# Performance work log

Measured on AMD Instinct MI355X. Metric: run time of the kernel, lower is better.

Reference implementation:

```python
import jax, jax.numpy as jnp
import numpy as np

B, S, D_IN, D_OUT = 8, 2048, 4096, 4096
RANK, N_ADAPTERS = 16, 8


def setup_inputs() -> dict:
    key = jax.random.key(0)
    k = jax.random.split(key, 6)
    x = jax.random.normal(k[0], (B, S, D_IN), dtype=jnp.float32)
    W = jax.random.normal(k[1], (D_OUT, D_IN), dtype=jnp.float32) * 0.02
    bias = jax.random.normal(k[2], (D_OUT,), dtype=jnp.float32) * 0.02
    lora_a = jax.random.normal(k[3], (N_ADAPTERS, RANK, D_IN), dtype=jnp.float32) * 0.02
    lora_b = jax.random.normal(k[4], (N_ADAPTERS, D_OUT, RANK), dtype=jnp.float32) * 0.02
    adapter_indices = jax.random.randint(k[5], (B,), 0, N_ADAPTERS, dtype=jnp.int64)
    return {"x": x, "W": W, "bias": bias, "lora_a": lora_a,
            "lora_b": lora_b, "adapter_indices": adapter_indices}


def reference(x, W, bias, lora_a, lora_b, adapter_indices):
    # Base linear: y = x @ W.T + bias
    base = jnp.einsum('bsi,oi->bso', x, W) + bias
    # Per-batch-element adapter gather (adapter index is shared across the seq dim)
    a = lora_a[adapter_indices]            # [B, r, D_in]
    b = lora_b[adapter_indices]            # [B, D_out, r]
    inter = jnp.einsum('bsi,bri->bsr', x, a)      # x_group @ a_i.T
    lora_out = jnp.einsum('bsr,bor->bso', inter, b)  # intermediate @ b_i.T
    return base + lora_out
```

## Files before the change

### kernel.cpp

```cpp
#include <hip/hip_runtime.h>


#define DIN     4096
#define DOUT    4096
#define RANK    16
#define M_DIM   16384
#define K_DIM   DIN
#define N_DIM   DOUT
#define BK      64
#define NT      (K_DIM / BK)
#define LDS_BYTES 131072

typedef __attribute__((ext_vector_type(8))) short  short8;
typedef __attribute__((ext_vector_type(4))) float  floatx4;
typedef __attribute__((ext_vector_type(4))) unsigned int uintx4;

__device__ __forceinline__ unsigned short f2bf(float f) {
  union { float f; unsigned int u; } v; v.f = f;
  return (unsigned short)((v.u + 0x7FFFu + ((v.u >> 16) & 1u)) >> 16);
}
__device__ __forceinline__ unsigned int pk2(float a, float b) {
  return (unsigned int)f2bf(a) | ((unsigned int)f2bf(b) << 16);
}

__device__ __forceinline__ int load_adapter(const int* __restrict__ p, int b) {
  bool i64 = (p[1] == 0) & (p[3] == 0) & (p[5] == 0) & (p[7] == 0);
  return i64 ? p[2 * b] : p[b];
}

__device__ __forceinline__ void async16(const unsigned short* g, void* s) {
  __builtin_amdgcn_global_load_lds(
      (const __attribute__((address_space(1))) void*)g,
      (__attribute__((address_space(3))) void*)s, 16, 0, 0);
}

__global__ __launch_bounds__(256) void conv_stream(const float* __restrict__ w,
                                                   unsigned short* __restrict__ wbf) {
  size_t base = ((size_t)blockIdx.x * 256 + threadIdx.x) * 8;
  const floatx4* src = (const floatx4*)(w + base);
  floatx4 f0 = __builtin_nontemporal_load(src);
  floatx4 f1 = __builtin_nontemporal_load(src + 1);
  uintx4 p;
  p.x = pk2(f0.x, f0.y); p.y = pk2(f0.z, f0.w);
  p.z = pk2(f1.x, f1.y); p.w = pk2(f1.z, f1.w);
  *(uintx4*)(wbf + base) = p;
}

__global__ __launch_bounds__(256) void inter16(
    const unsigned short* __restrict__ xbf,
    const float* __restrict__ lora_a,
    const int* __restrict__ adapters,
    float* __restrict__ inter) {
  __shared__ floatx4 red[4][64];
  const int tid = threadIdx.x, wave = tid >> 6, lane = tid & 63;
  const int fr = lane & 15, fq = lane >> 4;
  const int row0 = blockIdx.x * 16;
  const int adapter = load_adapter(adapters, row0 >> 11);
  const unsigned short* xp = xbf + (size_t)(row0 + fr) * DIN;
  const float* ap = lora_a + ((size_t)adapter * RANK + fr) * DIN;
  floatx4 acc = {};
  const int kbeg = blockIdx.y * 2048 + wave * 512;
#pragma unroll 2
  for (int k0 = kbeg; k0 < kbeg + 512; k0 += 32) {
    const int k = k0 + fq * 8;
    short8 xf = *(const short8*)(xp + k);
    floatx4 b0 = *(const floatx4*)(ap + k);
    floatx4 b1 = *(const floatx4*)(ap + k + 4);
    uintx4 bpk;
    bpk.x = pk2(b0.x, b0.y); bpk.y = pk2(b0.z, b0.w);
    bpk.z = pk2(b1.x, b1.y); bpk.w = pk2(b1.z, b1.w);
    acc = __builtin_amdgcn_mfma_f32_16x16x32_bf16(xf, *(short8*)&bpk, acc, 0, 0, 0);
  }
  red[wave][lane] = acc;
  __syncthreads();
  if (wave == 0) {
    floatx4 s = red[0][lane] + red[1][lane] + red[2][lane] + red[3][lane];
#pragma unroll
    for (int j = 0; j < 4; ++j)
      atomicAdd(&inter[(size_t)(row0 + fq * 4 + j) * RANK + fr], s[j]);
  }
}

#define PHASE_END() do {                                    \
    __builtin_amdgcn_sched_barrier(0);                      \
    __builtin_amdgcn_s_barrier();                           \
    __builtin_amdgcn_sched_barrier(0); } while (0)

__global__ __launch_bounds__(512, 2) void gemm256(
    const unsigned short* __restrict__ A,
    const unsigned short* __restrict__ Bw,
    const float* __restrict__ bias,
    const float* __restrict__ inter,
    const float* __restrict__ lora_b,
    const int* __restrict__ adapters,
    float* __restrict__ out) {
  extern __shared__ char lds[];
  const int tid  = threadIdx.x;
  const int lane = tid & 63, wave = tid >> 6;
  const int wm = wave >> 2, wn = wave & 3;

  const int wg   = ((int)blockIdx.x & 7) * 128 + ((int)blockIdx.x >> 3);
  const int row0 = (wg >> 4) * 256;
  const int col0 = (wg & 15) * 256;

  const int sg = (lane & 7) ^ (lane >> 3);
  const int sr = wave * 16 + (lane >> 3);
  const unsigned short* pA0 = A  + (size_t)(row0 + sr) * K_DIM + sg * 8;
  const unsigned short* pB0 = Bw + (size_t)(col0 + sr) * K_DIM + sg * 8;
  char* const dA0 = lds + wave * 2048;

#define STG_A(h, kt, buf) do {                                            \
    const unsigned short* _p = pA0 + (size_t)(h) * 128 * K_DIM + (kt) * BK; \
    char* _d = dA0 + (buf) * 65536 + (h) * 16384;                         \
    async16(_p, _d);                                                      \
    async16(_p + (size_t)8 * K_DIM, _d + 1024); } while (0)
#define STG_B(h, kt, buf) do {                                            \
    const unsigned short* _p = pB0 + (size_t)(h) * 128 * K_DIM + (kt) * BK; \
    char* _d = dA0 + 32768 + (buf) * 65536 + (h) * 16384;                 \
    async16(_p, _d);                                                      \
    async16(_p + (size_t)8 * K_DIM, _d + 1024); } while (0)

  const int fr = lane & 15, fq = lane >> 4;
  const int swz = (fr & 7) << 4;
  const int kb0 = (fq * 16) ^ swz;
  const int kb1 = (64 + fq * 16) ^ swz;
  const int ar = wm * 64 + fr;
  const int br = wn * 32 + fr;

  floatx4 acc[8][4] = {};
  short8 a[4][2], bl[2][2], bh[2][2];

  STG_A(0, 0, 0); STG_B(0, 0, 0); STG_B(1, 0, 0); STG_A(1, 0, 0);
  STG_A(0, 1, 1); STG_B(0, 1, 1); STG_B(1, 1, 1);
  asm volatile("s_waitcnt vmcnt(6)" ::: "memory");
  __builtin_amdgcn_sched_barrier(0);
  __builtin_amdgcn_s_barrier();
  __builtin_amdgcn_sched_barrier(0);

  for (int t = 0; t < NT; ++t) {
    const int buf = t & 1, nbuf = buf ^ 1;
    const char* ab = lds + buf * 65536;
    const char* bb = ab + 32768;
#pragma unroll
    for (int mt = 0; mt < 4; ++mt) {
      a[mt][0] = *(const short8*)(ab + (ar + mt * 16) * 128 + kb0);
      a[mt][1] = *(const short8*)(ab + (ar + mt * 16) * 128 + kb1);
    }
#pragma unroll
    for (int nt = 0; nt < 2; ++nt) {
      bl[nt][0] = *(const short8*)(bb + (br + nt * 16) * 128 + kb0);
      bl[nt][1] = *(const short8*)(bb + (br + nt * 16) * 128 + kb1);
    }
    if (t + 1 < NT) STG_A(1, t + 1, nbuf);
    __builtin_amdgcn_s_setprio(1);
#pragma unroll
    for (int mt = 0; mt < 4; ++mt)
#pragma unroll
      for (int nt = 0; nt < 2; ++nt) {
        acc[mt][nt] = __builtin_amdgcn_mfma_f32_16x16x32_bf16(a[mt][0], bl[nt][0], acc[mt][nt], 0, 0, 0);
        acc[mt][nt] = __builtin_amdgcn_mfma_f32_16x16x32_bf16(a[mt][1], bl[nt][1], acc[mt][nt], 0, 0, 0);
      }
    __builtin_amdgcn_s_setprio(0);
    PHASE_END();
#pragma unroll
    for (int nt = 0; nt < 2; ++nt) {
      bh[nt][0] = *(const short8*)(bb + (128 + br + nt * 16) * 128 + kb0);
      bh[nt][1] = *(const short8*)(bb + (128 + br + nt * 16) * 128 + kb1);
    }
    if (t + 2 < NT) STG_A(0, t + 2, buf);
    __builtin_amdgcn_s_setprio(1);
#pragma unroll
    for (int mt = 0; mt < 4; ++mt)
#pragma unroll
      for (int nt = 0; nt < 2; ++nt) {
        acc[mt][2 + nt] = __builtin_amdgcn_mfma_f32_16x16x32_bf16(a[mt][0], bh[nt][0], acc[mt][2 + nt], 0, 0, 0);
        acc[mt][2 + nt] = __builtin_amdgcn_mfma_f32_16x16x32_bf16(a[mt][1], bh[nt][1], acc[mt][2 + nt], 0, 0, 0);
      }
    __builtin_amdgcn_s_setprio(0);
    PHASE_END();
#pragma unroll
    for (int mt = 0; mt < 4; ++mt) {
      a[mt][0] = *(const short8*)(ab + (128 + ar + mt * 16) * 128 + kb0);
      a[mt][1] = *(const short8*)(ab + (128 + ar + mt * 16) * 128 + kb1);
    }
    if (t + 2 < NT) STG_B(0, t + 2, buf);
    __builtin_amdgcn_s_setprio(1);
#pragma unroll
    for (int mt = 0; mt < 4; ++mt)
#pragma unroll
      for (int nt = 0; nt < 2; ++nt) {
        acc[4 + mt][nt] = __builtin_amdgcn_mfma_f32_16x16x32_bf16(a[mt][0], bl[nt][0], acc[4 + mt][nt], 0, 0, 0);
        acc[4 + mt][nt] = __builtin_amdgcn_mfma_f32_16x16x32_bf16(a[mt][1], bl[nt][1], acc[4 + mt][nt], 0, 0, 0);
      }
    __builtin_amdgcn_s_setprio(0);
    PHASE_END();
    if (t + 2 < NT) STG_B(1, t + 2, buf);
    __builtin_amdgcn_s_setprio(1);
#pragma unroll
    for (int mt = 0; mt < 4; ++mt)
#pragma unroll
      for (int nt = 0; nt < 2; ++nt) {
        acc[4 + mt][2 + nt] = __builtin_amdgcn_mfma_f32_16x16x32_bf16(a[mt][0], bh[nt][0], acc[4 + mt][2 + nt], 0, 0, 0);
        acc[4 + mt][2 + nt] = __builtin_amdgcn_mfma_f32_16x16x32_bf16(a[mt][1], bh[nt][1], acc[4 + mt][2 + nt], 0, 0, 0);
      }
    __builtin_amdgcn_s_setprio(0);
    __builtin_amdgcn_sched_barrier(0);
    if (t + 2 < NT) {
      asm volatile("s_waitcnt vmcnt(6)" ::: "memory");
    } else {
      asm volatile("s_waitcnt vmcnt(0)" ::: "memory");
    }
    __builtin_amdgcn_sched_barrier(0);
    __builtin_amdgcn_s_barrier();
    __builtin_amdgcn_sched_barrier(0);
  }

  __syncthreads();
  const int adapter = load_adapter(adapters, row0 >> 11);
  {
    const int r = tid & 255;
    const float* src = (tid < 256)
        ? (inter + (size_t)(row0 + r) * RANK)
        : (lora_b + ((size_t)adapter * N_DIM + (col0 + r)) * RANK);
    char* dst = lds + ((tid < 256) ? 0 : 32768) + r * 128;
    const floatx4 v0 = ((const floatx4*)src)[0];
    const floatx4 v1 = ((const floatx4*)src)[1];
    const floatx4 v2 = ((const floatx4*)src)[2];
    const floatx4 v3 = ((const floatx4*)src)[3];
    uintx4 p0, p1;
    p0.x = pk2(v0.x, v0.y); p0.y = pk2(v0.z, v0.w);
    p0.z = pk2(v1.x, v1.y); p0.w = pk2(v1.z, v1.w);
    p1.x = pk2(v2.x, v2.y); p1.y = pk2(v2.z, v2.w);
    p1.z = pk2(v3.x, v3.y); p1.w = pk2(v3.z, v3.w);
    const int sw = (r & 7) << 4;
    *(uintx4*)(dst + (0  ^ sw)) = p0;
    *(uintx4*)(dst + (16 ^ sw)) = p1;
    uintx4 z = {0u, 0u, 0u, 0u};
    *(uintx4*)(dst + (32 ^ sw)) = z;
    *(uintx4*)(dst + (48 ^ sw)) = z;
  }
  __syncthreads();
  {
    short8 la[8], lb[4];
#pragma unroll
    for (int mt = 0; mt < 8; ++mt) {
      const int rl = (mt < 4 ? wm * 64 + mt * 16 : 128 + wm * 64 + (mt - 4) * 16) + fr;
      la[mt] = *(const short8*)(lds + rl * 128 + ((fq * 16) ^ swz));
    }
#pragma unroll
    for (int nt = 0; nt < 4; ++nt) {
      const int cl = (nt < 2 ? wn * 32 + nt * 16 : 128 + wn * 32 + (nt - 2) * 16) + fr;
      lb[nt] = *(const short8*)(lds + 32768 + cl * 128 + ((fq * 16) ^ swz));
    }
#pragma unroll
    for (int mt = 0; mt < 8; ++mt)
#pragma unroll
      for (int nt = 0; nt < 4; ++nt)
        acc[mt][nt] = __builtin_amdgcn_mfma_f32_16x16x32_bf16(la[mt], lb[nt], acc[mt][nt], 0, 0, 0);
  }

#pragma unroll
  for (int nt = 0; nt < 4; ++nt) {
    const int col = col0 + (nt < 2 ? wn * 32 + nt * 16 : 128 + wn * 32 + (nt - 2) * 16) + fr;
    const float bv = bias[col];
#pragma unroll
    for (int mt = 0; mt < 8; ++mt) {
      const int row = row0 + (mt < 4 ? wm * 64 + mt * 16 : 128 + wm * 64 + (mt - 4) * 16) + fq * 4;
      float* op = out + (size_t)row * N_DIM + col;
#pragma unroll
      for (int j = 0; j < 4; ++j)
        __builtin_nontemporal_store(acc[mt][nt][j] + bv, op + (size_t)j * N_DIM);
    }
  }
}

extern "C" void kernel_launch(void* const* d_in, const int* in_sizes, int n_in,
                              void* d_out, int out_size, void* d_ws, size_t ws_size,
                              hipStream_t stream) {
  const float* x      = (const float*)d_in[0];
  const float* W      = (const float*)d_in[1];
  const float* bias   = (const float*)d_in[2];
  const float* lora_a = (const float*)d_in[3];
  const float* lora_b = (const float*)d_in[4];
  const int*   aidx   = (const int*)d_in[5];
  float* out = (float*)d_out;

  const size_t xbf_bytes = (size_t)M_DIM * DIN * 2;
  const size_t wbf_bytes = (size_t)N_DIM * DIN * 2;
  unsigned short* xbf = (unsigned short*)d_ws;
  unsigned short* wbf = (unsigned short*)((char*)d_ws + xbf_bytes);
  float* inter = (float*)((char*)d_ws + xbf_bytes + wbf_bytes);

  static bool attr_set = false;
  if (!attr_set) {
    (void)hipFuncSetAttribute((const void*)gemm256,
                              hipFuncAttributeMaxDynamicSharedMemorySize, LDS_BYTES);
    attr_set = true;
  }

  conv_stream<<<dim3((size_t)N_DIM * DIN / (256 * 8)), dim3(256), 0, stream>>>(W, wbf);
  conv_stream<<<dim3((size_t)M_DIM * DIN / (256 * 8)), dim3(256), 0, stream>>>(x, xbf);
  (void)hipMemsetAsync(inter, 0, (size_t)M_DIM * RANK * sizeof(float), stream);
  inter16<<<dim3(M_DIM / 16, 2), dim3(256), 0, stream>>>(xbf, lora_a, aidx, inter);
  gemm256<<<dim3(1024), dim3(512), LDS_BYTES, stream>>>(
      xbf, wbf, bias, inter, lora_b, aidx, out);
}
```

Measured before the change: 918.0 us.

## Merge four MFMA phases into two and load all B fragments upfront

The per-K-tile inner loop goes from four phases (each loading A or B half-fragments and issuing 16 MFMAs) to two phases of 32 MFMAs. All four B fragments are loaded at the start, and the three remaining async global-to-LDS stages are issued together in the second phase. This cuts the number of phase barriers and LDS read stalls per tile. In exchange it raises register pressure for B fragments and bunches global loads, giving coarser interleaving of loads with compute.

```diff
diff --git a/kernel.cpp b/kernel.cpp
--- a/kernel.cpp
+++ b/kernel.cpp
@@ -128,7 +128,7 @@
   const int br = wn * 32 + fr;
 
   floatx4 acc[8][4] = {};
-  short8 a[4][2], bl[2][2], bh[2][2];
+  short8 a[4][2], b[4][2];
 
   STG_A(0, 0, 0); STG_B(0, 0, 0); STG_B(1, 0, 0); STG_A(1, 0, 0);
   STG_A(0, 1, 1); STG_B(0, 1, 1); STG_B(1, 1, 1);
@@ -148,60 +148,35 @@
     }
 #pragma unroll
     for (int nt = 0; nt < 2; ++nt) {
-      bl[nt][0] = *(const short8*)(bb + (br + nt * 16) * 128 + kb0);
-      bl[nt][1] = *(const short8*)(bb + (br + nt * 16) * 128 + kb1);
+      b[nt][0]     = *(const short8*)(bb + (br + nt * 16) * 128 + kb0);
+      b[nt][1]     = *(const short8*)(bb + (br + nt * 16) * 128 + kb1);
+      b[2 + nt][0] = *(const short8*)(bb + (128 + br + nt * 16) * 128 + kb0);
+      b[2 + nt][1] = *(const short8*)(bb + (128 + br + nt * 16) * 128 + kb1);
     }
     if (t + 1 < NT) STG_A(1, t + 1, nbuf);
     __builtin_amdgcn_s_setprio(1);
 #pragma unroll
     for (int mt = 0; mt < 4; ++mt)
 #pragma unroll
-      for (int nt = 0; nt < 2; ++nt) {
-        acc[mt][nt] = __builtin_amdgcn_mfma_f32_16x16x32_bf16(a[mt][0], bl[nt][0], acc[mt][nt], 0, 0, 0);
-        acc[mt][nt] = __builtin_amdgcn_mfma_f32_16x16x32_bf16(a[mt][1], bl[nt][1], acc[mt][nt], 0, 0, 0);
+      for (int nt = 0; nt < 4; ++nt) {
+        acc[mt][nt] = __builtin_amdgcn_mfma_f32_16x16x32_bf16(a[mt][0], b[nt][0], acc[mt][nt], 0, 0, 0);
+        acc[mt][nt] = __builtin_amdgcn_mfma_f32_16x16x32_bf16(a[mt][1], b[nt][1], acc[mt][nt], 0, 0, 0);
       }
     __builtin_amdgcn_s_setprio(0);
     PHASE_END();
 #pragma unroll
-    for (int nt = 0; nt < 2; ++nt) {
-      bh[nt][0] = *(const short8*)(bb + (128 + br + nt * 16) * 128 + kb0);
-      bh[nt][1] = *(const short8*)(bb + (128 + br + nt * 16) * 128 + kb1);
-    }
-    if (t + 2 < NT) STG_A(0, t + 2, buf);
-    __builtin_amdgcn_s_setprio(1);
-#pragma unroll
-    for (int mt = 0; mt < 4; ++mt)
-#pragma unroll
-      for (int nt = 0; nt < 2; ++nt) {
-        acc[mt][2 + nt] = __builtin_amdgcn_mfma_f32_16x16x32_bf16(a[mt][0], bh[nt][0], acc[mt][2 + nt], 0, 0, 0);
-        acc[mt][2 + nt] = __builtin_amdgcn_mfma_f32_16x16x32_bf16(a[mt][1], bh[nt][1], acc[mt][2 + nt], 0, 0, 0);
-      }
-    __builtin_amdgcn_s_setprio(0);
-    PHASE_END();
-#pragma unroll
     for (int mt = 0; mt < 4; ++mt) {
       a[mt][0] = *(const short8*)(ab + (128 + ar + mt * 16) * 128 + kb0);
       a[mt][1] = *(const short8*)(ab + (128 + ar + mt * 16) * 128 + kb1);
     }
-    if (t + 2 < NT) STG_B(0, t + 2, buf);
+    if (t + 2 < NT) { STG_A(0, t + 2, buf); STG_B(0, t + 2, buf); STG_B(1, t + 2, buf); }
     __builtin_amdgcn_s_setprio(1);
 #pragma unroll
     for (int mt = 0; mt < 4; ++mt)
 #pragma unroll
-      for (int nt = 0; nt < 2; ++nt) {
-        acc[4 + mt][nt] = __builtin_amdgcn_mfma_f32_16x16x32_bf16(a[mt][0], bl[nt][0], acc[4 + mt][nt], 0, 0, 0);
-        acc[4 + mt][nt] = __builtin_amdgcn_mfma_f32_16x16x32_bf16(a[mt][1], bl[nt][1], acc[4 + mt][nt], 0, 0, 0);
-      }
-    __builtin_amdgcn_s_setprio(0);
-    PHASE_END();
-    if (t + 2 < NT) STG_B(1, t + 2, buf);
-    __builtin_amdgcn_s_setprio(1);
-#pragma unroll
-    for (int mt = 0; mt < 4; ++mt)
-#pragma unroll
-      for (int nt = 0; nt < 2; ++nt) {
-        acc[4 + mt][2 + nt] = __builtin_amdgcn_mfma_f32_16x16x32_bf16(a[mt][0], bh[nt][0], acc[4 + mt][2 + nt], 0, 0, 0);
-        acc[4 + mt][2 + nt] = __builtin_amdgcn_mfma_f32_16x16x32_bf16(a[mt][1], bh[nt][1], acc[4 + mt][2 + nt], 0, 0, 0);
+      for (int nt = 0; nt < 4; ++nt) {
+        acc[4 + mt][nt] = __builtin_amdgcn_mfma_f32_16x16x32_bf16(a[mt][0], b[nt][0], acc[4 + mt][nt], 0, 0, 0);
+        acc[4 + mt][nt] = __builtin_amdgcn_mfma_f32_16x16x32_bf16(a[mt][1], b[nt][1], acc[4 + mt][nt], 0, 0, 0);
       }
     __builtin_amdgcn_s_setprio(0);
     __builtin_amdgcn_sched_barrier(0);
```

Measured after the change: 911.6 us. No clear change (-0.7%).
